# Kernel optimization log

Measured on AMD Instinct MI355X. Metric: run time of the kernel, lower is better.

The kernel has to match this reference:

```python
import jax, jax.numpy as jnp
import numpy as np

HID = 128   # Config.hidden_dim
K = 16      # kNN neighbors in TempEdgeConv
BIG = 1e9


def _glu(x, wl, bl, wg, bg):
    return (x @ wl + bl) * jax.nn.sigmoid(x @ wg + bg)


def _temp_edge_conv(h, t, w, b, k):
    # h: [G,n,d] node features, t: [G,n,1] temporal key feature
    # dynamic kNN graph on temporal distance within each graph
    d = jnp.abs(t - jnp.swapaxes(t, 1, 2))                  # [G,n,n]
    n = h.shape[1]
    d = d + jnp.eye(n, dtype=h.dtype) * BIG                  # exclude self
    _, idx = jax.lax.top_k(-d, k)                            # [G,n,k]
    hj = jax.vmap(lambda hg, ig: hg[ig])(h, idx)             # [G,n,k,d] gather
    hi = jnp.broadcast_to(h[:, :, None, :], hj.shape)
    e = jnp.concatenate([hi, hj - hi], axis=-1)              # [G,n,k,2d]
    e = e @ w + b                                            # edge MLP
    return jnp.max(e, axis=2)                                # max aggregation


def setup_inputs():
    key = jax.random.key(0)
    ks = jax.random.split(key, 18)
    G, n, IN, H = 64, 1024, 17, HID
    N = G * n
    feat = IN - 1                  # 16
    temb = H // 4                  # 32

    def lin(k1, i, o):
        ka, kb = jax.random.split(k1)
        return (jax.random.normal(ka, (i, o), jnp.float32) / np.sqrt(i),
                jax.random.normal(kb, (o,), jnp.float32) * 0.01)

    x = jax.random.normal(ks[0], (N, IN), jnp.float32)
    batch = jnp.repeat(jnp.arange(G, dtype=jnp.int32), n)
    te_w, te_b = lin(ks[1], 1, temb)
    ig_lw, ig_lb = lin(ks[2], feat + temb, H)
    ig_gw, ig_gb = lin(ks[3], feat + temb, H)
    c1_w, c1_b = lin(ks[4], 2 * H, H)
    c2_w, c2_b = lin(ks[5], 2 * H, H)
    fg_lw, fg_lb = lin(ks[6], 4 * H, H)
    fg_gw, fg_gb = lin(ks[7], 4 * H, H)
    out_w, out_b = lin(ks[8], H, 2)
    return {"x": x, "te_w": te_w, "te_b": te_b,
            "ig_lw": ig_lw, "ig_lb": ig_lb, "ig_gw": ig_gw, "ig_gb": ig_gb,
            "c1_w": c1_w, "c1_b": c1_b, "c2_w": c2_w, "c2_b": c2_b,
            "fg_lw": fg_lw, "fg_lb": fg_lb, "fg_gw": fg_gw, "fg_gb": fg_gb,
            "out_w": out_w, "out_b": out_b,
            "batch": batch, "num_graphs": 64}


def reference(x, te_w, te_b, ig_lw, ig_lb, ig_gw, ig_gb,
              c1_w, c1_b, c2_w, c2_b, fg_lw, fg_lb, fg_gw, fg_gb,
              out_w, out_b, batch, num_graphs):
    G = int(num_graphs)
    N = x.shape[0]
    n = N // G   # equal-sized graphs (batch = repeat(arange(G), n))
    key_feat = x[:, :1]                       # key_feature_idx == 0
    feats = x[:, 1:]
    t_emb = key_feat @ te_w + te_b            # time encoder [N, H//4]
    h = _glu(jnp.concatenate([feats, t_emb], axis=-1),
             ig_lw, ig_lb, ig_gw, ig_gb)      # [N, H] (dropout = identity, eval)
    h = h.reshape(G, n, HID)
    t = key_feat.reshape(G, n, 1)
    x1 = jax.nn.relu(_temp_edge_conv(h, t, c1_w, c1_b, K))   # [G,n,H]
    x2 = jax.nn.relu(_temp_edge_conv(x1, t, c2_w, c2_b, K))  # [G,n,H]
    comb = jnp.concatenate([x1, x2], axis=-1)                # [G,n,2H]
    pooled = jnp.concatenate([comb.max(axis=1), comb.mean(axis=1)], axis=-1)  # [G,4H]
    logits = _glu(pooled, fg_lw, fg_lb, fg_gw, fg_gb) @ out_w + out_b
    return jax.nn.log_softmax(logits, axis=-1)
```

## Files before the change

kernel.cpp:

```cpp
#include <hip/hip_runtime.h>
#include <math.h>

#define NN 65536
#define NG 64
#define NPG 1024
#define HID 128
#define KNN 16
#define BINF 1e30f
#define BWS 272

typedef unsigned long long ull;
typedef _Float16 f16;
typedef _Float16 f16x8 __attribute__((ext_vector_type(8)));
typedef float f32x4 __attribute__((ext_vector_type(4)));

__global__ __launch_bounds__(1024) void k_topk(
    const float* __restrict__ x, int* __restrict__ sidxg,
    short* __restrict__ nbroff,
    const float* __restrict__ ig_lw, const float* __restrict__ ig_gw,
    const float* __restrict__ c1_w, const float* __restrict__ c2_w,
    f16* __restrict__ gfrag, f16* __restrict__ f1, f16* __restrict__ f2) {
    __shared__ ull key[1024];
    __shared__ float st[1024];
    __shared__ int sidx[1024];
    int g = blockIdx.x;
    if (g >= NG) {
        int gid = (g - NG) * 1024 + threadIdx.x;
        if (gid < 16384) {
            int i = gid & 7, lane = (gid >> 3) & 63, nt = (gid >> 9) & 7;
            int kt = (gid >> 12) & 1, mat = gid >> 13;
            int k = kt * 32 + ((lane >> 4) << 3) + i;
            int c = nt * 16 + (lane & 15);
            float v = 0.0f;
            if (k < 48) v = (mat ? ig_gw : ig_lw)[k * 128 + c];
            gfrag[gid] = (f16)v;
        } else {
            int g2 = gid - 16384;
            int buf = g2 >> 15;
            int rem = g2 & 32767;
            int mat = rem >> 14;
            int r2 = rem & 16383;
            int i = r2 & 7, lane = (r2 >> 3) & 63, nt = (r2 >> 9) & 7, kt = (r2 >> 12) & 3;
            int k = kt * 32 + ((lane >> 4) << 3) + i;
            int c = nt * 16 + (lane & 15);
            const float* cw = buf ? c2_w : c1_w;
            float top = cw[k * 128 + c];
            float bot = cw[(128 + k) * 128 + c];
            float v = mat ? bot : (top - bot);
            (buf ? f2 : f1)[rem] = (f16)v;
        }
        return;
    }
    int i = threadIdx.x;
    float t = x[(size_t)(g * NPG + i) * 17];
    unsigned ub = __float_as_uint(t);
    ub = (ub & 0x80000000u) ? ~ub : (ub | 0x80000000u);
    ull kk = ((ull)ub << 32) | (unsigned)i;

    for (int k = 2; k <= 1024; k <<= 1) {
        for (int j = k >> 1; j > 0; j >>= 1) {
            ull pv;
            if (j >= 64) {
                key[i] = kk;
                __syncthreads();
                pv = key[i ^ j];
                __syncthreads();
            } else {
                pv = __shfl_xor(kk, j, 64);
            }
            bool up = ((i & k) == 0);
            bool low = ((i & j) == 0);
            ull mn = kk < pv ? kk : pv;
            ull mx = kk < pv ? pv : kk;
            kk = (up == low) ? mn : mx;
        }
    }
    int oi = (int)(kk & 0xffffffffu);
    st[i] = x[(size_t)(g * NPG + oi) * 17];
    sidx[i] = oi;
    sidxg[g * NPG + i] = g * NPG + oi;
    __syncthreads();

    float tt = st[i];
    int L = i - 1, R = i + 1;
    short* out = nbroff + (size_t)(g * NPG + i) * KNN;
#pragma unroll
    for (int q = 0; q < KNN; q++) {
        float dl = (L >= 0)   ? (tt - st[L]) : BINF;
        float dr = (R < NPG) ? (st[R] - tt) : BINF;
        bool left;
        if (dl < dr) left = true;
        else if (dr < dl) left = false;
        else left = (sidx[L] < sidx[R]);
        int jr;
        if (left) { jr = L; L--; }
        else      { jr = R; R++; }
        out[q] = (short)((jr - i) * BWS);
    }
}

__global__ __launch_bounds__(256) void k_fuse1(
    const float* __restrict__ x, const float* __restrict__ te_w,
    const float* __restrict__ te_b, const f16x8* __restrict__ gfrag,
    const float* __restrict__ bl, const float* __restrict__ bg,
    const int* __restrict__ sidxg, const f16x8* __restrict__ wfrag,
    const float* __restrict__ cb, f16* __restrict__ A, f16* __restrict__ B) {
    __shared__ f16x8 XL[4 * 2 * 64];
    __shared__ f16 ht[64 * 128];
    int tid = threadIdx.x;
    int r0 = blockIdx.x * 64;
#pragma unroll
    for (int p = 0; p < 2; p++) {
        int idx = tid + p * 256;
        int row = idx >> 3, kq = idx & 7;
        int node = sidxg[r0 + row];
        f16x8 h;
        if (kq < 2) {
            const float* xr = x + (size_t)node * 17 + 1 + kq * 8;
#pragma unroll
            for (int i = 0; i < 8; i++) h[i] = (f16)xr[i];
        } else if (kq < 6) {
            float t = x[(size_t)node * 17];
            int j0 = (kq - 2) * 8;
#pragma unroll
            for (int i = 0; i < 8; i++) h[i] = (f16)fmaf(t, te_w[j0 + i], te_b[j0 + i]);
        } else {
#pragma unroll
            for (int i = 0; i < 8; i++) h[i] = (f16)0.0f;
        }
        int mf = row >> 4, kt = kq >> 2, lane = ((kq & 3) << 4) | (row & 15);
        XL[(mf * 2 + kt) * 64 + lane] = h;
    }
    __syncthreads();
    int w = tid >> 6, lane = tid & 63;
    f32x4 acc[2][2][4];
#pragma unroll
    for (int o = 0; o < 2; o++)
#pragma unroll
        for (int j = 0; j < 2; j++)
#pragma unroll
            for (int mf = 0; mf < 4; mf++) acc[o][j][mf] = (f32x4){0.f, 0.f, 0.f, 0.f};
#pragma unroll 1
    for (int kt = 0; kt < 2; kt++) {
        f16x8 wf0[2], wf1[2], xa[4];
#pragma unroll
        for (int j = 0; j < 2; j++) {
            wf0[j] = gfrag[((0 * 2 + kt) * 8 + (w * 2 + j)) * 64 + lane];
            wf1[j] = gfrag[((1 * 2 + kt) * 8 + (w * 2 + j)) * 64 + lane];
        }
#pragma unroll
        for (int mf = 0; mf < 4; mf++) xa[mf] = XL[(mf * 2 + kt) * 64 + lane];
#pragma unroll
        for (int mf = 0; mf < 4; mf++)
#pragma unroll
            for (int j = 0; j < 2; j++) {
                acc[0][j][mf] = __builtin_amdgcn_mfma_f32_16x16x32_f16(xa[mf], wf0[j], acc[0][j][mf], 0, 0, 0);
                acc[1][j][mf] = __builtin_amdgcn_mfma_f32_16x16x32_f16(xa[mf], wf1[j], acc[1][j][mf], 0, 0, 0);
            }
    }
#pragma unroll
    for (int j = 0; j < 2; j++) {
        int col = w * 32 + j * 16 + (lane & 15);
        float bbl = bl[col], bbg = bg[col];
#pragma unroll
        for (int mf = 0; mf < 4; mf++) {
            int rloc = mf * 16 + ((lane >> 4) << 2);
#pragma unroll
            for (int q = 0; q < 4; q++) {
                float lin = acc[0][j][mf][q] + bbl;
                float gat = acc[1][j][mf][q] + bbg;
                int row = rloc + q;
                ht[(row * 128 + col) ^ ((row & 7) << 3)] = (f16)(lin / (1.0f + expf(-gat)));
            }
        }
    }
    __syncthreads();
#pragma unroll
    for (int o = 0; o < 2; o++)
#pragma unroll
        for (int j = 0; j < 2; j++)
#pragma unroll
            for (int mf = 0; mf < 4; mf++) acc[o][j][mf] = (f32x4){0.f, 0.f, 0.f, 0.f};
    int row16 = lane & 15, kslot = lane >> 4;
    int swz = (row16 & 7) << 3;
#pragma unroll 1
    for (int kt = 0; kt < 4; kt++) {
        f16x8 wf0[2], wf1[2], xa[4];
#pragma unroll
        for (int j = 0; j < 2; j++) {
            wf0[j] = wfrag[((0 * 4 + kt) * 8 + (w * 2 + j)) * 64 + lane];
            wf1[j] = wfrag[((1 * 4 + kt) * 8 + (w * 2 + j)) * 64 + lane];
        }
#pragma unroll
        for (int mf = 0; mf < 4; mf++)
            xa[mf] = *(const f16x8*)&ht[((mf * 16 + row16) * 128 + kt * 32 + kslot * 8) ^ swz];
#pragma unroll
        for (int mf = 0; mf < 4; mf++)
#pragma unroll
            for (int j = 0; j < 2; j++) {
                acc[0][j][mf] = __builtin_amdgcn_mfma_f32_16x16x32_f16(xa[mf], wf0[j], acc[0][j][mf], 0, 0, 0);
                acc[1][j][mf] = __builtin_amdgcn_mfma_f32_16x16x32_f16(xa[mf], wf1[j], acc[1][j][mf], 0, 0, 0);
            }
    }
#pragma unroll
    for (int j = 0; j < 2; j++) {
        int col = w * 32 + j * 16 + (lane & 15);
        float bias = cb[col];
#pragma unroll
        for (int mf = 0; mf < 4; mf++) {
            int rbase = r0 + mf * 16 + ((lane >> 4) << 2);
#pragma unroll
            for (int q = 0; q < 4; q++) {
                A[(size_t)(rbase + q) * 128 + col] = (f16)(acc[0][j][mf][q] + bias);
                B[(size_t)(rbase + q) * 128 + col] = (f16)acc[1][j][mf][q];
            }
        }
    }
}

__global__ __launch_bounds__(512) void k_megac2(
    const f16* __restrict__ A1, const f16* __restrict__ B1,
    const short* __restrict__ nbroff, const f16x8* __restrict__ wfrag,
    const float* __restrict__ cb,
    float* __restrict__ partM1, float* __restrict__ partS1,
    float* __restrict__ partM2, float* __restrict__ partS2) {
    __shared__ char SM[76800];
    char* bw  = SM;
    char* b2  = SM;
    f16*  x1t = (f16*)(SM + 34816);
    char* a2  = SM + 59392;
    float* redM1 = (float*)(SM + 59392);
    float* redS1 = (float*)(SM + 63488);
    float* redM2 = (float*)(SM + 34816);
    float* redS2 = (float*)(SM + 38912);

    int tid = threadIdx.x;
    int bx = blockIdx.x;
    int r0 = bx * 64;
    int r0loc = (bx & 15) * 64;
    int gbase = r0 - r0loc;

#pragma unroll
    for (int p = 0; p < 4; p++) {
        int idx = tid + p * 512;
        int row = idx >> 4, kq = idx & 15;
        int gl = r0loc - 32 + row;
        f16x8 v;
#pragma unroll
        for (int i = 0; i < 8; i++) v[i] = (f16)0.0f;
        if (gl >= 0 && gl < NPG)
            v = *(const f16x8*)(B1 + (size_t)(gbase + gl) * 128 + kq * 8);
        *(f16x8*)(bw + row * BWS + kq * 16) = v;
    }
    __syncthreads();

    int w = tid >> 6, lane = tid & 63;
    int rquad = lane >> 4;
    int c0 = (lane & 15) * 8;

    f16x8 pmv;
    float ps[8];
#pragma unroll
    for (int i = 0; i < 8; i++) { pmv[i] = (f16)(-INFINITY); ps[i] = 0.f; }
#pragma unroll 1
    for (int rr = 0; rr < 3; rr++) {
        int row = w * 12 + rr * 4 + rquad;
        int gl = r0loc - 16 + row;
        f16x8 ou;
#pragma unroll
        for (int i = 0; i < 8; i++) ou[i] = (f16)0.0f;
        if (gl >= 0 && gl < NPG) {
            int grow = gbase + gl;
            const int4* op = (const int4*)(nbroff + (size_t)grow * KNN);
            int4 oa = op[0], ob = op[1];
            short ow[16];
            *(int4*)ow = oa; *(int4*)(ow + 8) = ob;
            f16x8 av = *(const f16x8*)(A1 + (size_t)grow * 128 + c0);
            f16x8 m;
#pragma unroll
            for (int i = 0; i < 8; i++) m[i] = (f16)(-INFINITY);
            const char* base = bw + (row + 16) * BWS + c0 * 2;
#pragma unroll
            for (int q = 0; q < 16; q++) {
                f16x8 bv = *(const f16x8*)(base + (int)ow[q]);
                m = __builtin_elementwise_max(m, bv);
            }
            f16x8 z = {(f16)0, (f16)0, (f16)0, (f16)0, (f16)0, (f16)0, (f16)0, (f16)0};
            ou = __builtin_elementwise_max(av + m, z);
            if ((row >= 16) && (row < 80)) {
                pmv = __builtin_elementwise_max(pmv, ou);
#pragma unroll
                for (int i = 0; i < 8; i++) ps[i] += (float)ou[i];
            }
        }
        int idx = (row * 128 + c0) ^ ((row & 7) << 3);
        *(f16x8*)&x1t[idx] = ou;
    }
    float pm[8];
#pragma unroll
    for (int i = 0; i < 8; i++) pm[i] = (float)pmv[i];
#pragma unroll
    for (int i = 0; i < 8; i++) {
        pm[i] = fmaxf(pm[i], __shfl_xor(pm[i], 16));
        pm[i] = fmaxf(pm[i], __shfl_xor(pm[i], 32));
        ps[i] += __shfl_xor(ps[i], 16);
        ps[i] += __shfl_xor(ps[i], 32);
    }
    if (rquad == 0) {
#pragma unroll
        for (int i = 0; i < 8; i++) {
            redM1[w * 128 + c0 + i] = pm[i];
            redS1[w * 128 + c0 + i] = ps[i];
        }
    }
    __syncthreads();
    if (tid < 128) {
        float M = -BINF, S = 0.f;
#pragma unroll
        for (int w2 = 0; w2 < 8; w2++) {
            M = fmaxf(M, redM1[w2 * 128 + tid]);
            S += redS1[w2 * 128 + tid];
        }
        partM1[(size_t)bx * 128 + tid] = M;
        partS1[(size_t)bx * 128 + tid] = S;
    }
    __syncthreads();

    f32x4 acc[2][6];
#pragma unroll
    for (int o = 0; o < 2; o++)
#pragma unroll
        for (int mf = 0; mf < 6; mf++) acc[o][mf] = (f32x4){0.f, 0.f, 0.f, 0.f};
    int row16 = lane & 15, kslot = lane >> 4;
    int swz = (row16 & 7) << 3;
#pragma unroll 1
    for (int kt = 0; kt < 4; kt++) {
        f16x8 wf0, wf1, xa[6];
        wf0 = wfrag[((0 * 4 + kt) * 8 + w) * 64 + lane];
        wf1 = wfrag[((1 * 4 + kt) * 8 + w) * 64 + lane];
#pragma unroll
        for (int mf = 0; mf < 6; mf++)
            xa[mf] = *(const f16x8*)&x1t[((mf * 16 + row16) * 128 + kt * 32 + kslot * 8) ^ swz];
#pragma unroll
        for (int mf = 0; mf < 6; mf++) {
            acc[0][mf] = __builtin_amdgcn_mfma_f32_16x16x32_f16(xa[mf], wf0, acc[0][mf], 0, 0, 0);
            acc[1][mf] = __builtin_amdgcn_mfma_f32_16x16x32_f16(xa[mf], wf1, acc[1][mf], 0, 0, 0);
        }
    }
    {
        int col = w * 16 + (lane & 15);
        float bias = cb[col];
#pragma unroll
        for (int mf = 0; mf < 6; mf++) {
            int rloc = mf * 16 + ((lane >> 4) << 2);
#pragma unroll
            for (int q = 0; q < 4; q++) {
                int hrow = rloc + q;
                *(f16*)(b2 + hrow * BWS + col * 2) = (f16)acc[1][mf][q];
                if (hrow >= 16 && hrow < 80)
                    *(f16*)(a2 + (hrow - 16) * BWS + col * 2) = (f16)(acc[0][mf][q] + bias);
            }
        }
    }
    __syncthreads();

#pragma unroll
    for (int i = 0; i < 8; i++) { pmv[i] = (f16)(-INFINITY); ps[i] = 0.f; }
#pragma unroll 1
    for (int rr = 0; rr < 2; rr++) {
        int rl = w * 8 + rr * 4 + rquad;
        int grow = r0 + rl;
        const int4* op = (const int4*)(nbroff + (size_t)grow * KNN);
        int4 oa = op[0], ob = op[1];
        short ow[16];
        *(int4*)ow = oa; *(int4*)(ow + 8) = ob;
        f16x8 av = *(const f16x8*)(a2 + rl * BWS + c0 * 2);
        f16x8 m;
#pragma unroll
        for (int i = 0; i < 8; i++) m[i] = (f16)(-INFINITY);
        const char* base = b2 + (rl + 16) * BWS + c0 * 2;
#pragma unroll
        for (int q = 0; q < 16; q++) {
            f16x8 bv = *(const f16x8*)(base + (int)ow[q]);
            m = __builtin_elementwise_max(m, bv);
        }
        f16x8 z = {(f16)0, (f16)0, (f16)0, (f16)0, (f16)0, (f16)0, (f16)0, (f16)0};
        f16x8 v = __builtin_elementwise_max(av + m, z);
        pmv = __builtin_elementwise_max(pmv, v);
#pragma unroll
        for (int i = 0; i < 8; i++) ps[i] += (float)v[i];
    }
#pragma unroll
    for (int i = 0; i < 8; i++) pm[i] = (float)pmv[i];
#pragma unroll
    for (int i = 0; i < 8; i++) {
        pm[i] = fmaxf(pm[i], __shfl_xor(pm[i], 16));
        pm[i] = fmaxf(pm[i], __shfl_xor(pm[i], 32));
        ps[i] += __shfl_xor(ps[i], 16);
        ps[i] += __shfl_xor(ps[i], 32);
    }
    __syncthreads();
    if (rquad == 0) {
#pragma unroll
        for (int i = 0; i < 8; i++) {
            redM2[w * 128 + c0 + i] = pm[i];
            redS2[w * 128 + c0 + i] = ps[i];
        }
    }
    __syncthreads();
    if (tid < 128) {
        float M = -BINF, S = 0.f;
#pragma unroll
        for (int w2 = 0; w2 < 8; w2++) {
            M = fmaxf(M, redM2[w2 * 128 + tid]);
            S += redS2[w2 * 128 + tid];
        }
        partM2[(size_t)bx * 128 + tid] = M;
        partS2[(size_t)bx * 128 + tid] = S;
    }
}

__global__ __launch_bounds__(256) void k_final(const float* __restrict__ partM1,
                                               const float* __restrict__ partS1,
                                               const float* __restrict__ partM2,
                                               const float* __restrict__ partS2,
                                               const float* __restrict__ fg_lw,
                                               const float* __restrict__ fg_lb,
                                               const float* __restrict__ fg_gw,
                                               const float* __restrict__ fg_gb,
                                               const float* __restrict__ out_w,
                                               const float* __restrict__ out_b,
                                               float* __restrict__ out) {
    __shared__ float pooled[512];
    __shared__ float linv[128], gatev[128];
    __shared__ float gluv[128];
    __shared__ float lg[2];
    int g = blockIdx.x, tid = threadIdx.x;

    const float* pM = (tid < 128) ? partM1 : partM2;
    const float* pS = (tid < 128) ? partS1 : partS2;
    int cc = tid & 127;
    float mx = -BINF, sm = 0.0f;
    for (int ch = 0; ch < 16; ch++) {
        mx = fmaxf(mx, pM[(size_t)(g * 16 + ch) * 128 + cc]);
        sm += pS[(size_t)(g * 16 + ch) * 128 + cc];
    }
    pooled[tid] = mx;
    pooled[256 + tid] = sm * (1.0f / 1024.0f);
    __syncthreads();

    float acc = 0.0f;
    if (tid < 128) {
        for (int k = 0; k < 512; k++) acc = fmaf(pooled[k], fg_lw[k * 128 + tid], acc);
        linv[tid] = acc + fg_lb[tid];
    } else {
        int c = tid - 128;
        for (int k = 0; k < 512; k++) acc = fmaf(pooled[k], fg_gw[k * 128 + c], acc);
        gatev[c] = acc + fg_gb[c];
    }
    __syncthreads();
    if (tid < 128) gluv[tid] = linv[tid] / (1.0f + expf(-gatev[tid]));
    __syncthreads();
    if (tid < 2) {
        float s = out_b[tid];
        for (int c = 0; c < 128; c++) s = fmaf(gluv[c], out_w[c * 2 + tid], s);
        lg[tid] = s;
    }
    __syncthreads();
    if (tid < 2) {
        float m = fmaxf(lg[0], lg[1]);
        float lse = m + logf(expf(lg[0] - m) + expf(lg[1] - m));
        out[g * 2 + tid] = lg[tid] - lse;
    }
}

extern "C" void kernel_launch(void* const* d_in, const int* in_sizes, int n_in,
                              void* d_out, int out_size, void* d_ws, size_t ws_size,
                              hipStream_t stream) {
    const float* x     = (const float*)d_in[0];
    const float* te_w  = (const float*)d_in[1];
    const float* te_b  = (const float*)d_in[2];
    const float* ig_lw = (const float*)d_in[3];
    const float* ig_lb = (const float*)d_in[4];
    const float* ig_gw = (const float*)d_in[5];
    const float* ig_gb = (const float*)d_in[6];
    const float* c1_w  = (const float*)d_in[7];
    const float* c1_b  = (const float*)d_in[8];
    const float* c2_w  = (const float*)d_in[9];
    const float* c2_b  = (const float*)d_in[10];
    const float* fg_lw = (const float*)d_in[11];
    const float* fg_lb = (const float*)d_in[12];
    const float* fg_gw = (const float*)d_in[13];
    const float* fg_gb = (const float*)d_in[14];
    const float* out_w = (const float*)d_in[15];
    const float* out_b = (const float*)d_in[16];
    float* out = (float*)d_out;

    char* p = (char*)d_ws;
    const size_t T16 = (size_t)NN * HID * sizeof(f16);
    f16* A1 = (f16*)p; p += T16;
    f16* B1 = (f16*)p; p += T16;
    int* sidxg = (int*)p;            p += (size_t)NN * 4;
    short* nbroff = (short*)p;       p += (size_t)NN * KNN * 2;
    float* partM1 = (float*)p;       p += (size_t)1024 * 128 * 4;
    float* partS1 = (float*)p;       p += (size_t)1024 * 128 * 4;
    float* partM2 = (float*)p;       p += (size_t)1024 * 128 * 4;
    float* partS2 = (float*)p;       p += (size_t)1024 * 128 * 4;
    f16* gfrag = (f16*)p;            p += 16384 * 2;
    f16* f1 = (f16*)p;               p += 32768 * 2;
    f16* f2 = (f16*)p;               p += 32768 * 2;

    k_topk<<<NG + 80, 1024, 0, stream>>>(x, sidxg, nbroff, ig_lw, ig_gw,
                                         c1_w, c2_w, gfrag, f1, f2);
    k_fuse1<<<NN / 64, 256, 0, stream>>>(x, te_w, te_b, (const f16x8*)gfrag,
                                         ig_lb, ig_gb, sidxg, (const f16x8*)f1,
                                         c1_b, A1, B1);
    k_megac2<<<NN / 64, 512, 0, stream>>>(A1, B1, nbroff, (const f16x8*)f2,
                                          c2_b, partM1, partS1, partM2, partS2);
    k_final<<<NG, 256, 0, stream>>>(partM1, partS1, partM2, partS2,
                                    fg_lw, fg_lb, fg_gw, fg_gb, out_w, out_b, out);
}
```

Baseline: 103.3 us.

## Fuse input GLU and conv1 projection into mega kernel with halo recompute

Merges the input-GLU and first edge-conv projection kernel into the conv kernel. Each 64-row block now recomputes the GLU and both conv1 projections for a 128-row window (a 32-row halo on each side) directly in shared memory. This removes the global round trip of the A1/B1 fp16 tensors and one kernel launch, and neighbor offsets are also staged in LDS. In exchange it doubles the input-stage MFMA work per block and grows LDS to about 105KB, which lowers occupancy.

```diff
diff --git a/kernel.cpp b/kernel.cpp
--- a/kernel.cpp
+++ b/kernel.cpp
@@ -99,140 +99,26 @@
     }
 }
 
-__global__ __launch_bounds__(256) void k_fuse1(
+__global__ __launch_bounds__(512) void k_mega(
     const float* __restrict__ x, const float* __restrict__ te_w,
     const float* __restrict__ te_b, const f16x8* __restrict__ gfrag,
     const float* __restrict__ bl, const float* __restrict__ bg,
-    const int* __restrict__ sidxg, const f16x8* __restrict__ wfrag,
-    const float* __restrict__ cb, f16* __restrict__ A, f16* __restrict__ B) {
-    __shared__ f16x8 XL[4 * 2 * 64];
-    __shared__ f16 ht[64 * 128];
-    int tid = threadIdx.x;
-    int r0 = blockIdx.x * 64;
-#pragma unroll
-    for (int p = 0; p < 2; p++) {
-        int idx = tid + p * 256;
-        int row = idx >> 3, kq = idx & 7;
-        int node = sidxg[r0 + row];
-        f16x8 h;
-        if (kq < 2) {
-            const float* xr = x + (size_t)node * 17 + 1 + kq * 8;
-#pragma unroll
-            for (int i = 0; i < 8; i++) h[i] = (f16)xr[i];
-        } else if (kq < 6) {
-            float t = x[(size_t)node * 17];
-            int j0 = (kq - 2) * 8;
-#pragma unroll
-            for (int i = 0; i < 8; i++) h[i] = (f16)fmaf(t, te_w[j0 + i], te_b[j0 + i]);
-        } else {
-#pragma unroll
-            for (int i = 0; i < 8; i++) h[i] = (f16)0.0f;
-        }
-        int mf = row >> 4, kt = kq >> 2, lane = ((kq & 3) << 4) | (row & 15);
-        XL[(mf * 2 + kt) * 64 + lane] = h;
-    }
-    __syncthreads();
-    int w = tid >> 6, lane = tid & 63;
-    f32x4 acc[2][2][4];
-#pragma unroll
-    for (int o = 0; o < 2; o++)
-#pragma unroll
-        for (int j = 0; j < 2; j++)
-#pragma unroll
-            for (int mf = 0; mf < 4; mf++) acc[o][j][mf] = (f32x4){0.f, 0.f, 0.f, 0.f};
-#pragma unroll 1
-    for (int kt = 0; kt < 2; kt++) {
-        f16x8 wf0[2], wf1[2], xa[4];
-#pragma unroll
-        for (int j = 0; j < 2; j++) {
-            wf0[j] = gfrag[((0 * 2 + kt) * 8 + (w * 2 + j)) * 64 + lane];
-            wf1[j] = gfrag[((1 * 2 + kt) * 8 + (w * 2 + j)) * 64 + lane];
-        }
-#pragma unroll
-        for (int mf = 0; mf < 4; mf++) xa[mf] = XL[(mf * 2 + kt) * 64 + lane];
-#pragma unroll
-        for (int mf = 0; mf < 4; mf++)
-#pragma unroll
-            for (int j = 0; j < 2; j++) {
-                acc[0][j][mf] = __builtin_amdgcn_mfma_f32_16x16x32_f16(xa[mf], wf0[j], acc[0][j][mf], 0, 0, 0);
-                acc[1][j][mf] = __builtin_amdgcn_mfma_f32_16x16x32_f16(xa[mf], wf1[j], acc[1][j][mf], 0, 0, 0);
-            }
-    }
-#pragma unroll
-    for (int j = 0; j < 2; j++) {
-        int col = w * 32 + j * 16 + (lane & 15);
-        float bbl = bl[col], bbg = bg[col];
-#pragma unroll
-        for (int mf = 0; mf < 4; mf++) {
-            int rloc = mf * 16 + ((lane >> 4) << 2);
-#pragma unroll
-            for (int q = 0; q < 4; q++) {
-                float lin = acc[0][j][mf][q] + bbl;
-                float gat = acc[1][j][mf][q] + bbg;
-                int row = rloc + q;
-                ht[(row * 128 + col) ^ ((row & 7) << 3)] = (f16)(lin / (1.0f + expf(-gat)));
-            }
-        }
-    }
-    __syncthreads();
-#pragma unroll
-    for (int o = 0; o < 2; o++)
-#pragma unroll
-        for (int j = 0; j < 2; j++)
-#pragma unroll
-            for (int mf = 0; mf < 4; mf++) acc[o][j][mf] = (f32x4){0.f, 0.f, 0.f, 0.f};
-    int row16 = lane & 15, kslot = lane >> 4;
-    int swz = (row16 & 7) << 3;
-#pragma unroll 1
-    for (int kt = 0; kt < 4; kt++) {
-        f16x8 wf0[2], wf1[2], xa[4];
-#pragma unroll
-        for (int j = 0; j < 2; j++) {
-            wf0[j] = wfrag[((0 * 4 + kt) * 8 + (w * 2 + j)) * 64 + lane];
-            wf1[j] = wfrag[((1 * 4 + kt) * 8 + (w * 2 + j)) * 64 + lane];
-        }
-#pragma unroll
-        for (int mf = 0; mf < 4; mf++)
-            xa[mf] = *(const f16x8*)&ht[((mf * 16 + row16) * 128 + kt * 32 + kslot * 8) ^ swz];
-#pragma unroll
-        for (int mf = 0; mf < 4; mf++)
-#pragma unroll
-            for (int j = 0; j < 2; j++) {
-                acc[0][j][mf] = __builtin_amdgcn_mfma_f32_16x16x32_f16(xa[mf], wf0[j], acc[0][j][mf], 0, 0, 0);
-                acc[1][j][mf] = __builtin_amdgcn_mfma_f32_16x16x32_f16(xa[mf], wf1[j], acc[1][j][mf], 0, 0, 0);
-            }
-    }
-#pragma unroll
-    for (int j = 0; j < 2; j++) {
-        int col = w * 32 + j * 16 + (lane & 15);
-        float bias = cb[col];
-#pragma unroll
-        for (int mf = 0; mf < 4; mf++) {
-            int rbase = r0 + mf * 16 + ((lane >> 4) << 2);
-#pragma unroll
-            for (int q = 0; q < 4; q++) {
-                A[(size_t)(rbase + q) * 128 + col] = (f16)(acc[0][j][mf][q] + bias);
-                B[(size_t)(rbase + q) * 128 + col] = (f16)acc[1][j][mf][q];
-            }
-        }
-    }
-}
-
-__global__ __launch_bounds__(512) void k_megac2(
-    const f16* __restrict__ A1, const f16* __restrict__ B1,
-    const short* __restrict__ nbroff, const f16x8* __restrict__ wfrag,
-    const float* __restrict__ cb,
+    const int* __restrict__ sidxg, const short* __restrict__ nbroff,
+    const f16x8* __restrict__ w1frag, const float* __restrict__ c1b,
+    const f16x8* __restrict__ w2frag, const float* __restrict__ c2b,
     float* __restrict__ partM1, float* __restrict__ partS1,
     float* __restrict__ partM2, float* __restrict__ partS2) {
-    __shared__ char SM[76800];
-    char* bw  = SM;
-    char* b2  = SM;
-    f16*  x1t = (f16*)(SM + 34816);
-    char* a2  = SM + 59392;
-    float* redM1 = (float*)(SM + 59392);
-    float* redS1 = (float*)(SM + 63488);
-    float* redM2 = (float*)(SM + 34816);
-    float* redS2 = (float*)(SM + 38912);
+    __shared__ char SM[104960];
+    f16*  ht  = (f16*)SM;
+    f16*  x1t = (f16*)SM;
+    char* a1  = SM + 32768;
+    char* a2  = SM + 32768;
+    char* b1  = SM + 58880;
+    f16x8* XL = (f16x8*)(SM + 58880);
+    char* b2  = SM + 58880;
+    float* redM = (float*)(SM + 93696);
+    float* redS = (float*)(SM + 97792);
+    short* nbrL = (short*)(SM + 101888);
 
     int tid = threadIdx.x;
     int bx = blockIdx.x;
@@ -241,20 +127,112 @@
     int gbase = r0 - r0loc;
 
 #pragma unroll
-    for (int p = 0; p < 4; p++) {
+    for (int p = 0; p < 2; p++) {
         int idx = tid + p * 512;
-        int row = idx >> 4, kq = idx & 15;
+        int row = idx >> 3, kq = idx & 7;
         int gl = r0loc - 32 + row;
-        f16x8 v;
-#pragma unroll
-        for (int i = 0; i < 8; i++) v[i] = (f16)0.0f;
+        f16x8 h;
+#pragma unroll
+        for (int i = 0; i < 8; i++) h[i] = (f16)0.0f;
+        if (gl >= 0 && gl < NPG) {
+            int node = sidxg[gbase + gl];
+            if (kq < 2) {
+                const float* xr = x + (size_t)node * 17 + 1 + kq * 8;
+#pragma unroll
+                for (int i = 0; i < 8; i++) h[i] = (f16)xr[i];
+            } else if (kq < 6) {
+                float t = x[(size_t)node * 17];
+                int j0 = (kq - 2) * 8;
+#pragma unroll
+                for (int i = 0; i < 8; i++) h[i] = (f16)fmaf(t, te_w[j0 + i], te_b[j0 + i]);
+            }
+        }
+        int mf = row >> 4, kt = kq >> 2, lane = ((kq & 3) << 4) | (row & 15);
+        XL[(mf * 2 + kt) * 64 + lane] = h;
+    }
+    if (tid < 192) {
+        int row = tid >> 1, half = tid & 1;
+        int gl = r0loc - 16 + row;
+        int4 v = {0, 0, 0, 0};
         if (gl >= 0 && gl < NPG)
-            v = *(const f16x8*)(B1 + (size_t)(gbase + gl) * 128 + kq * 8);
-        *(f16x8*)(bw + row * BWS + kq * 16) = v;
+            v = ((const int4*)(nbroff + (size_t)(gbase + gl) * KNN))[half];
+        ((int4*)nbrL)[tid] = v;
     }
     __syncthreads();
 
     int w = tid >> 6, lane = tid & 63;
+    int row16 = lane & 15, kslot = lane >> 4;
+    int swz = (row16 & 7) << 3;
+    int col = w * 16 + row16;
+
+    f32x4 acc[2][8];
+#pragma unroll
+    for (int o = 0; o < 2; o++)
+#pragma unroll
+        for (int mf = 0; mf < 8; mf++) acc[o][mf] = (f32x4){0.f, 0.f, 0.f, 0.f};
+#pragma unroll 1
+    for (int kt = 0; kt < 2; kt++) {
+        f16x8 wf0 = gfrag[((0 * 2 + kt) * 8 + w) * 64 + lane];
+        f16x8 wf1 = gfrag[((1 * 2 + kt) * 8 + w) * 64 + lane];
+        f16x8 xa[8];
+#pragma unroll
+        for (int mf = 0; mf < 8; mf++) xa[mf] = XL[(mf * 2 + kt) * 64 + lane];
+#pragma unroll
+        for (int mf = 0; mf < 8; mf++) {
+            acc[0][mf] = __builtin_amdgcn_mfma_f32_16x16x32_f16(xa[mf], wf0, acc[0][mf], 0, 0, 0);
+            acc[1][mf] = __builtin_amdgcn_mfma_f32_16x16x32_f16(xa[mf], wf1, acc[1][mf], 0, 0, 0);
+        }
+    }
+    {
+        float bbl = bl[col], bbg = bg[col];
+#pragma unroll
+        for (int mf = 0; mf < 8; mf++) {
+            int rloc = mf * 16 + (kslot << 2);
+#pragma unroll
+            for (int q = 0; q < 4; q++) {
+                float lin = acc[0][mf][q] + bbl;
+                float gat = acc[1][mf][q] + bbg;
+                int row = rloc + q;
+                ht[(row * 128 + col) ^ ((row & 7) << 3)] = (f16)(lin / (1.0f + expf(-gat)));
+            }
+        }
+    }
+    __syncthreads();
+
+#pragma unroll
+    for (int o = 0; o < 2; o++)
+#pragma unroll
+        for (int mf = 0; mf < 8; mf++) acc[o][mf] = (f32x4){0.f, 0.f, 0.f, 0.f};
+#pragma unroll 1
+    for (int kt = 0; kt < 4; kt++) {
+        f16x8 wf0 = w1frag[((0 * 4 + kt) * 8 + w) * 64 + lane];
+        f16x8 wf1 = w1frag[((1 * 4 + kt) * 8 + w) * 64 + lane];
+        f16x8 xa[8];
+#pragma unroll
+        for (int mf = 0; mf < 8; mf++)
+            xa[mf] = *(const f16x8*)&ht[((mf * 16 + row16) * 128 + kt * 32 + kslot * 8) ^ swz];
+#pragma unroll
+        for (int mf = 0; mf < 8; mf++) {
+            acc[0][mf] = __builtin_amdgcn_mfma_f32_16x16x32_f16(xa[mf], wf0, acc[0][mf], 0, 0, 0);
+            acc[1][mf] = __builtin_amdgcn_mfma_f32_16x16x32_f16(xa[mf], wf1, acc[1][mf], 0, 0, 0);
+        }
+    }
+    {
+        float bias = c1b[col];
+#pragma unroll
+        for (int mf = 0; mf < 8; mf++) {
+            int rloc = mf * 16 + (kslot << 2);
+#pragma unroll
+            for (int q = 0; q < 4; q++) {
+                int hrow = rloc + q;
+                *(f16*)(b1 + hrow * BWS + col * 2) = (f16)acc[1][mf][q];
+                if (hrow >= 16 && hrow < 112)
+                    *(f16*)(a1 + (hrow - 16) * BWS + col * 2) = (f16)(acc[0][mf][q] + bias);
+            }
+        }
+    }
+    __syncthreads();
+
     int rquad = lane >> 4;
     int c0 = (lane & 15) * 8;
 
@@ -270,16 +248,15 @@
 #pragma unroll
         for (int i = 0; i < 8; i++) ou[i] = (f16)0.0f;
         if (gl >= 0 && gl < NPG) {
-            int grow = gbase + gl;
-            const int4* op = (const int4*)(nbroff + (size_t)grow * KNN);
-            int4 oa = op[0], ob = op[1];
+            int4 oa = ((const int4*)nbrL)[row * 2];
+            int4 ob = ((const int4*)nbrL)[row * 2 + 1];
             short ow[16];
             *(int4*)ow = oa; *(int4*)(ow + 8) = ob;
-            f16x8 av = *(const f16x8*)(A1 + (size_t)grow * 128 + c0);
+            f16x8 av = *(const f16x8*)(a1 + row * BWS + c0 * 2);
             f16x8 m;
 #pragma unroll
             for (int i = 0; i < 8; i++) m[i] = (f16)(-INFINITY);
-            const char* base = bw + (row + 16) * BWS + c0 * 2;
+            const char* base = b1 + (row + 16) * BWS + c0 * 2;
 #pragma unroll
             for (int q = 0; q < 16; q++) {
                 f16x8 bv = *(const f16x8*)(base + (int)ow[q]);
@@ -309,8 +286,8 @@
     if (rquad == 0) {
 #pragma unroll
         for (int i = 0; i < 8; i++) {
-            redM1[w * 128 + c0 + i] = pm[i];
-            redS1[w * 128 + c0 + i] = ps[i];
+            redM[w * 128 + c0 + i] = pm[i];
+            redS[w * 128 + c0 + i] = ps[i];
         }
     }
     __syncthreads();
@@ -318,26 +295,22 @@
         float M = -BINF, S = 0.f;
 #pragma unroll
         for (int w2 = 0; w2 < 8; w2++) {
-            M = fmaxf(M, redM1[w2 * 128 + tid]);
-            S += redS1[w2 * 128 + tid];
+            M = fmaxf(M, redM[w2 * 128 + tid]);
+            S += redS[w2 * 128 + tid];
         }
         partM1[(size_t)bx * 128 + tid] = M;
         partS1[(size_t)bx * 128 + tid] = S;
     }
-    __syncthreads();
-
-    f32x4 acc[2][6];
+
 #pragma unroll
     for (int o = 0; o < 2; o++)
 #pragma unroll
         for (int mf = 0; mf < 6; mf++) acc[o][mf] = (f32x4){0.f, 0.f, 0.f, 0.f};
-    int row16 = lane & 15, kslot = lane >> 4;
-    int swz = (row16 & 7) << 3;
 #pragma unroll 1
     for (int kt = 0; kt < 4; kt++) {
-        f16x8 wf0, wf1, xa[6];
-        wf0 = wfrag[((0 * 4 + kt) * 8 + w) * 64 + lane];
-        wf1 = wfrag[((1 * 4 + kt) * 8 + w) * 64 + lane];
+        f16x8 wf0 = w2frag[((0 * 4 + kt) * 8 + w) * 64 + lane];
+        f16x8 wf1 = w2frag[((1 * 4 + kt) * 8 + w) * 64 + lane];
+        f16x8 xa[6];
 #pragma unroll
         for (int mf = 0; mf < 6; mf++)
             xa[mf] = *(const f16x8*)&x1t[((mf * 16 + row16) * 128 + kt * 32 + kslot * 8) ^ swz];
@@ -348,11 +321,10 @@
         }
     }
     {
-        int col = w * 16 + (lane & 15);
-        float bias = cb[col];
+        float bias = c2b[col];
 #pragma unroll
         for (int mf = 0; mf < 6; mf++) {
-            int rloc = mf * 16 + ((lane >> 4) << 2);
+            int rloc = mf * 16 + (kslot << 2);
 #pragma unroll
             for (int q = 0; q < 4; q++) {
                 int hrow = rloc + q;
@@ -369,9 +341,9 @@
 #pragma unroll 1
     for (int rr = 0; rr < 2; rr++) {
         int rl = w * 8 + rr * 4 + rquad;
-        int grow = r0 + rl;
-        const int4* op = (const int4*)(nbroff + (size_t)grow * KNN);
-        int4 oa = op[0], ob = op[1];
+        int nrow = rl + 16;
+        int4 oa = ((const int4*)nbrL)[nrow * 2];
+        int4 ob = ((const int4*)nbrL)[nrow * 2 + 1];
         short ow[16];
         *(int4*)ow = oa; *(int4*)(ow + 8) = ob;
         f16x8 av = *(const f16x8*)(a2 + rl * BWS + c0 * 2);
@@ -403,8 +375,8 @@
     if (rquad == 0) {
 #pragma unroll
         for (int i = 0; i < 8; i++) {
-            redM2[w * 128 + c0 + i] = pm[i];
-            redS2[w * 128 + c0 + i] = ps[i];
+            redM[w * 128 + c0 + i] = pm[i];
+            redS[w * 128 + c0 + i] = ps[i];
         }
     }
     __syncthreads();
@@ -412,8 +384,8 @@
         float M = -BINF, S = 0.f;
 #pragma unroll
         for (int w2 = 0; w2 < 8; w2++) {
-            M = fmaxf(M, redM2[w2 * 128 + tid]);
-            S += redS2[w2 * 128 + tid];
+            M = fmaxf(M, redM[w2 * 128 + tid]);
+            S += redS[w2 * 128 + tid];
         }
         partM2[(size_t)bx * 128 + tid] = M;
         partS2[(size_t)bx * 128 + tid] = S;
@@ -497,9 +469,6 @@
     float* out = (float*)d_out;
 
     char* p = (char*)d_ws;
-    const size_t T16 = (size_t)NN * HID * sizeof(f16);
-    f16* A1 = (f16*)p; p += T16;
-    f16* B1 = (f16*)p; p += T16;
     int* sidxg = (int*)p;            p += (size_t)NN * 4;
     short* nbroff = (short*)p;       p += (size_t)NN * KNN * 2;
     float* partM1 = (float*)p;       p += (size_t)1024 * 128 * 4;
@@ -512,11 +481,11 @@
 
     k_topk<<<NG + 80, 1024, 0, stream>>>(x, sidxg, nbroff, ig_lw, ig_gw,
                                          c1_w, c2_w, gfrag, f1, f2);
-    k_fuse1<<<NN / 64, 256, 0, stream>>>(x, te_w, te_b, (const f16x8*)gfrag,
-                                         ig_lb, ig_gb, sidxg, (const f16x8*)f1,
-                                         c1_b, A1, B1);
-    k_megac2<<<NN / 64, 512, 0, stream>>>(A1, B1, nbroff, (const f16x8*)f2,
-                                          c2_b, partM1, partS1, partM2, partS2);
+    k_mega<<<NN / 64, 512, 0, stream>>>(x, te_w, te_b, (const f16x8*)gfrag,
+                                        ig_lb, ig_gb, sidxg, nbroff,
+                                        (const f16x8*)f1, c1_b,
+                                        (const f16x8*)f2, c2_b,
+                                        partM1, partS1, partM2, partS2);
     k_final<<<NG, 256, 0, stream>>>(partM1, partS1, partM2, partS2,
                                     fg_lw, fg_lb, fg_gw, fg_gb, out_w, out_b, out);
 }
```

New measurement: 117.0 us. +13.2%, slower.
